# Performance work log

Hardware: AMD Instinct MI355X
Metric: run time of the kernel (lower is better)

## Reference

```python
import jax, jax.numpy as jnp
import numpy as np

HEADS = 8
DIM_HEAD = 64
LN_EPS = 1e-5


def _layernorm(x, gamma, beta):
    mu = jnp.mean(x, axis=-1, keepdims=True)
    var = jnp.var(x, axis=-1, keepdims=True)
    return (x - mu) * jax.lax.rsqrt(var + LN_EPS) * gamma + beta


def setup_inputs() -> dict:
    key = jax.random.key(0)
    ks = jax.random.split(key, 5)
    B, N, D = 1, 16384, 512
    return {
        "x": jax.random.normal(ks[0], (B, N, D), dtype=jnp.float32),
        "ln_gamma": jnp.ones((D,), dtype=jnp.float32),
        "ln_beta": jnp.zeros((D,), dtype=jnp.float32),
        "w_qkv": jax.random.normal(ks[1], (D, 3 * D), dtype=jnp.float32) * (D ** -0.5),
        "agent": jax.random.normal(ks[2], (HEADS, 512, DIM_HEAD), dtype=jnp.float32) * (DIM_HEAD ** -0.5),
        "w_out": jax.random.normal(ks[3], (D, D), dtype=jnp.float32) * (D ** -0.5),
        "b_out": jnp.zeros((D,), dtype=jnp.float32),
    }


def reference(x, ln_gamma, ln_beta, w_qkv, agent, w_out, b_out):
    # TransLayer: x + Mask_Agent_Attention(LayerNorm(x))
    B, N, D = x.shape
    xn = _layernorm(x, ln_gamma, ln_beta)

    qkv = xn @ w_qkv                                   # [B, N, 3D]
    q, k, v = jnp.split(qkv, 3, axis=-1)
    # [B, H, N, d]
    q = q.reshape(B, N, HEADS, DIM_HEAD).transpose(0, 2, 1, 3)
    k = k.reshape(B, N, HEADS, DIM_HEAD).transpose(0, 2, 1, 3)
    v = v.reshape(B, N, HEADS, DIM_HEAD).transpose(0, 2, 1, 3)

    scale = DIM_HEAD ** -0.5  # tem=0 -> classical 1/sqrt(d) scaling

    # agents aggregate values: softmax over keys  [B, H, A, N]
    attn1 = jax.nn.softmax(jnp.einsum('had,bhnd->bhan', agent, k) * scale, axis=-1)
    agent_v = jnp.einsum('bhan,bhnd->bhad', attn1, v)  # [B, H, A, d]

    # queries attend to agents: softmax over agents  [B, H, N, A]
    attn2 = jax.nn.softmax(jnp.einsum('bhnd,had->bhna', q, agent) * scale, axis=-1)
    out = jnp.einsum('bhna,bhad->bhnd', attn2, agent_v)  # [B, H, N, d]

    out = out + v  # residual=True: value residual inside attention
    out = out.transpose(0, 2, 1, 3).reshape(B, N, D)
    out = out @ w_out + b_out
    return x + out
```

## Files before the change

kernel.cpp:

```cpp
#include <hip/hip_runtime.h>
#include <stdint.h>

typedef unsigned short u16;
typedef __attribute__((ext_vector_type(8))) short bf16x8;
typedef __attribute__((ext_vector_type(4))) float f32x4;

__device__ __forceinline__ float bf2f(u16 u){
  union { uint32_t i; float f; } v; v.i = ((uint32_t)u) << 16; return v.f;
}
__device__ __forceinline__ u16 f2bf(float f){
  union { float fl; uint32_t i; } v; v.fl = f;
  uint32_t r = v.i + 0x7FFFu + ((v.i >> 16) & 1u);
  return (u16)(r >> 16);
}
__device__ __forceinline__ uint32_t cvt_pk_bf16(float lo, float hi){
  uint32_t r;
  asm("v_cvt_pk_bf16_f32 %0, %1, %2" : "=v"(r) : "v"(lo), "v"(hi));
  return r;
}
__device__ __forceinline__ f32x4 mfma16(bf16x8 a, bf16x8 b, f32x4 c){
  return __builtin_amdgcn_mfma_f32_16x16x32_bf16(a, b, c, 0, 0, 0);
}
__device__ __forceinline__ void gload16(const u16* g, u16* l){
  __builtin_amdgcn_global_load_lds((const __attribute__((address_space(1))) void*)g,
                                   (__attribute__((address_space(3))) void*)l, 16, 0, 0);
}

__global__ __launch_bounds__(256) void k_conv_bf(const float* __restrict__ in, u16* __restrict__ out, int n, float scale){
  int i = (blockIdx.x * 256 + threadIdx.x) * 4;
  if (i >= n) return;
  float4 v = *(const float4*)(in + i);
  ushort4 o; o.x=f2bf(v.x*scale); o.y=f2bf(v.y*scale); o.z=f2bf(v.z*scale); o.w=f2bf(v.w*scale);
  *(ushort4*)(out + i) = o;
}

__global__ __launch_bounds__(256) void k_transp(const float* __restrict__ in, u16* __restrict__ out, int R, int C){
  __shared__ u16 tile[64][68];
  int c0 = blockIdx.x * 64, r0 = blockIdx.y * 64;
  int tr = threadIdx.x >> 4;
  int tc = (threadIdx.x & 15) * 4;
  for (int rr = 0; rr < 4; rr++){
    int r = rr * 16 + tr;
    float4 v = *(const float4*)(in + (size_t)(r0 + r) * C + c0 + tc);
    ushort4 o; o.x=f2bf(v.x); o.y=f2bf(v.y); o.z=f2bf(v.z); o.w=f2bf(v.w);
    *(ushort4*)&tile[r][tc] = o;
  }
  __syncthreads();
  for (int rr = 0; rr < 4; rr++){
    int oc = rr * 16 + tr;
    ushort4 o;
    o.x = tile[tc+0][oc]; o.y = tile[tc+1][oc]; o.z = tile[tc+2][oc]; o.w = tile[tc+3][oc];
    *(ushort4*)(out + (size_t)(c0 + oc) * R + r0 + tc) = o;
  }
}

__global__ __launch_bounds__(256) void k_transp_v(const u16* __restrict__ qkv, u16* __restrict__ vT){
  __shared__ u16 tile[64][68];
  int n0 = blockIdx.x * 64;
  int c0 = blockIdx.y * 64;
  int tr = threadIdx.x >> 4;
  int tc = (threadIdx.x & 15) * 4;
  for (int rr = 0; rr < 4; rr++){
    int r = rr * 16 + tr;
    ushort4 v = *(const ushort4*)(qkv + (size_t)(n0 + r) * 1536 + 1024 + c0 + tc);
    *(ushort4*)&tile[r][tc] = v;
  }
  __syncthreads();
  for (int rr = 0; rr < 4; rr++){
    int oc = rr * 16 + tr;
    ushort4 o;
    o.x = tile[tc+0][oc]; o.y = tile[tc+1][oc]; o.z = tile[tc+2][oc]; o.w = tile[tc+3][oc];
    *(ushort4*)(vT + (size_t)(c0 + oc) * 16384 + n0 + tc) = o;
  }
}

__global__ __launch_bounds__(128) void k_ln(const float* __restrict__ x, const float* __restrict__ g,
                                            const float* __restrict__ b, u16* __restrict__ xn){
  int row = blockIdx.x;
  int t = threadIdx.x;
  float4 v = *(const float4*)(x + (size_t)row * 512 + t * 4);
  float s = v.x + v.y + v.z + v.w;
  float q = v.x*v.x + v.y*v.y + v.z*v.z + v.w*v.w;
  for (int o = 32; o > 0; o >>= 1){ s += __shfl_down(s, o); q += __shfl_down(q, o); }
  __shared__ float red[4];
  if ((t & 63) == 0){ red[(t >> 6) * 2] = s; red[(t >> 6) * 2 + 1] = q; }
  __syncthreads();
  float mu  = (red[0] + red[2]) * (1.0f/512.0f);
  float var = (red[1] + red[3]) * (1.0f/512.0f) - mu * mu;
  float rs = rsqrtf(var + 1e-5f);
  float4 gv = *(const float4*)(g + t * 4);
  float4 bv = *(const float4*)(b + t * 4);
  ushort4 o;
  o.x = f2bf((v.x - mu) * rs * gv.x + bv.x);
  o.y = f2bf((v.y - mu) * rs * gv.y + bv.y);
  o.z = f2bf((v.z - mu) * rs * gv.z + bv.z);
  o.w = f2bf((v.w - mu) * rs * gv.w + bv.w);
  *(ushort4*)(xn + (size_t)row * 512 + t * 4) = o;
}


__global__ __launch_bounds__(512) void k_gemm_qkv(const u16* __restrict__ A, const u16* __restrict__ Bt,
                                                  u16* __restrict__ C){
  __shared__ u16 aL[2][256 * 64];
  __shared__ u16 bL[2][128 * 64];
  int m0 = blockIdx.x * 256, n0 = blockIdx.y * 128;
  int t = threadIdx.x, w = t >> 6, l = t & 63;
  int wm = (w >> 1) * 64, wn = (w & 1) * 64;
  int lr = l & 15;
  int blkSrc = (l & 7) ^ ((l >> 3) & 7);
  const u16* gA = A  + (size_t)(m0 + w*8 + (l >> 3)) * 512 + blkSrc * 8;
  const u16* gB = Bt + (size_t)(n0 + w*8 + (l >> 3)) * 512 + blkSrc * 8;
  f32x4 acc[4][4];
  for (int i=0;i<4;i++) for (int j=0;j<4;j++) acc[i][j] = {0.f,0.f,0.f,0.f};

  auto stage = [&](int buf, int k0){
    #pragma unroll
    for (int p = 0; p < 4; p++)
      gload16(gA + (size_t)p*64*512 + k0, &aL[buf][(p*64 + w*8) * 64]);
    #pragma unroll
    for (int p = 0; p < 2; p++)
      gload16(gB + (size_t)p*64*512 + k0, &bL[buf][(p*64 + w*8) * 64]);
  };
  auto comp = [&](const u16* ab, const u16* bb){
    #pragma unroll
    for (int kk = 0; kk < 64; kk += 32){
      int xo = (((l >> 4) + (kk >> 3)) ^ (l & 7)) << 3;
      bf16x8 av[4], bv[4];
      #pragma unroll
      for (int mt=0;mt<4;mt++) av[mt] = *(const bf16x8*)&ab[(wm + mt*16 + lr)*64 + xo];
      #pragma unroll
      for (int nt=0;nt<4;nt++) bv[nt] = *(const bf16x8*)&bb[(wn + nt*16 + lr)*64 + xo];
      #pragma unroll
      for (int mt=0;mt<4;mt++)
        #pragma unroll
        for (int nt=0;nt<4;nt++)
          acc[mt][nt] = mfma16(av[mt], bv[nt], acc[mt][nt]);
    }
  };

  stage(0, 0);
  __syncthreads();
  #pragma unroll
  for (int tk = 0; tk < 8; tk++){
    int cur = tk & 1;
    if (tk < 7) stage(cur ^ 1, (tk + 1) * 64);
    comp(&aL[cur][0], &bL[cur][0]);
    __syncthreads();
  }

  int rr = (l >> 4) * 4, cc = l & 15;
  for (int mt=0;mt<4;mt++) for (int nt=0;nt<4;nt++)
    for (int j=0;j<4;j++){
      int r = m0 + wm + mt*16 + rr + j;
      int c = n0 + wn + nt*16 + cc;
      C[(size_t)r * 1536 + c] = f2bf(acc[mt][nt][j]);
    }
}

__global__ __launch_bounds__(512) void k_gemm_out(const u16* __restrict__ A, const u16* __restrict__ Bt,
                                                  const float* __restrict__ x, const float* __restrict__ bias,
                                                  float* __restrict__ y){
  __shared__ u16 aL[2][256 * 64];
  __shared__ u16 bL[2][128 * 64];
  int m0 = blockIdx.x * 256, n0 = blockIdx.y * 128;
  int t = threadIdx.x, w = t >> 6, l = t & 63;
  int wm = (w >> 1) * 64, wn = (w & 1) * 64;
  int lr = l & 15;
  int blkSrc = (l & 7) ^ ((l >> 3) & 7);
  const u16* gA = A  + (size_t)(m0 + w*8 + (l >> 3)) * 512 + blkSrc * 8;
  const u16* gB = Bt + (size_t)(n0 + w*8 + (l >> 3)) * 512 + blkSrc * 8;
  f32x4 acc[4][4];
  for (int i=0;i<4;i++) for (int j=0;j<4;j++) acc[i][j] = {0.f,0.f,0.f,0.f};

  auto stage = [&](int buf, int k0){
    #pragma unroll
    for (int p = 0; p < 4; p++)
      gload16(gA + (size_t)p*64*512 + k0, &aL[buf][(p*64 + w*8) * 64]);
    #pragma unroll
    for (int p = 0; p < 2; p++)
      gload16(gB + (size_t)p*64*512 + k0, &bL[buf][(p*64 + w*8) * 64]);
  };
  auto comp = [&](const u16* ab, const u16* bb){
    #pragma unroll
    for (int kk = 0; kk < 64; kk += 32){
      int xo = (((l >> 4) + (kk >> 3)) ^ (l & 7)) << 3;
      bf16x8 av[4], bv[4];
      #pragma unroll
      for (int mt=0;mt<4;mt++) av[mt] = *(const bf16x8*)&ab[(wm + mt*16 + lr)*64 + xo];
      #pragma unroll
      for (int nt=0;nt<4;nt++) bv[nt] = *(const bf16x8*)&bb[(wn + nt*16 + lr)*64 + xo];
      #pragma unroll
      for (int mt=0;mt<4;mt++)
        #pragma unroll
        for (int nt=0;nt<4;nt++)
          acc[mt][nt] = mfma16(av[mt], bv[nt], acc[mt][nt]);
    }
  };

  stage(0, 0);
  __syncthreads();
  #pragma unroll
  for (int tk = 0; tk < 8; tk++){
    int cur = tk & 1;
    if (tk < 7) stage(cur ^ 1, (tk + 1) * 64);
    comp(&aL[cur][0], &bL[cur][0]);
    __syncthreads();
  }

  int rr = (l >> 4) * 4, cc = l & 15;
  for (int mt=0;mt<4;mt++) for (int nt=0;nt<4;nt++)
    for (int j=0;j<4;j++){
      int r = m0 + wm + mt*16 + rr + j;
      int c = n0 + wn + nt*16 + cc;
      y[(size_t)r * 512 + c] = acc[mt][nt][j] + bias[c] + x[(size_t)r * 512 + c];
    }
}

__global__ __launch_bounds__(256) void k_agent_agg(const u16* __restrict__ agbf, const u16* __restrict__ qkv,
                                                   const u16* __restrict__ vT,
                                                   float* __restrict__ nump, float* __restrict__ denp){
  int L = blockIdx.x;
  int g = (L >> 6) * 8 + (L & 7);
  int m = (L >> 3) & 7;
  int h = g >> 4, ch = g & 15, a0 = m * 64;

  __shared__ u16 ag[64][72];
  __shared__ u16 kt[64][72];
  __shared__ u16 vt[64][72];
  __shared__ u16 pt[64][72];
  int t = threadIdx.x, w = t >> 6, l = t & 63;

  for (int i = 0; i < 2; i++){
    int flat = t + 256 * i;
    int r = flat >> 3, c = (flat & 7) * 8;
    *(uint4*)&ag[r][c] = *(const uint4*)(agbf + (size_t)(h * 512 + a0 + r) * 64 + c);
  }

  bf16x8 ones;
  for (int i = 0; i < 8; i++) ones[i] = (short)0x3F80;

  f32x4 acc2[4];
  for (int i=0;i<4;i++) acc2[i] = {0.f,0.f,0.f,0.f};
  f32x4 accd = {0.f,0.f,0.f,0.f};

  for (int sub = 0; sub < 16; sub++){
    int n0 = ch * 1024 + sub * 64;
    __syncthreads();
    {
      int flat = t;
      int r = flat >> 3, c = (flat & 7) * 8;
      *(uint4*)&kt[r][c] = *(const uint4*)(qkv + (size_t)(n0 + r) * 1536 + 512 + h * 64 + c);
      int flat2 = t + 256;
      int r2 = flat2 >> 3, c2 = (flat2 & 7) * 8;
      *(uint4*)&kt[r2][c2] = *(const uint4*)(qkv + (size_t)(n0 + r2) * 1536 + 512 + h * 64 + c2);
      *(uint4*)&vt[r][c]   = *(const uint4*)(vT + ((size_t)(h * 64 + r) << 14) + n0 + c);
      *(uint4*)&vt[r2][c2] = *(const uint4*)(vT + ((size_t)(h * 64 + r2) << 14) + n0 + c2);
    }
    __syncthreads();

    f32x4 s[4];
    for (int nt=0;nt<4;nt++) s[nt] = {0.f,0.f,0.f,0.f};
    for (int kk = 0; kk < 64; kk += 32){
      int kb = kk + (l >> 4) * 8;
      bf16x8 kf = *(const bf16x8*)&kt[w*16 + (l & 15)][kb];
      for (int nt=0;nt<4;nt++){
        bf16x8 af = *(const bf16x8*)&ag[nt*16 + (l & 15)][kb];
        s[nt] = mfma16(kf, af, s[nt]);
      }
    }
    int nb = w*16 + (l >> 4) * 4;
    for (int nt=0;nt<4;nt++){
      int a = nt*16 + (l & 15);
      uint32_t w0 = cvt_pk_bf16(__builtin_amdgcn_exp2f(s[nt][0]), __builtin_amdgcn_exp2f(s[nt][1]));
      uint32_t w1 = cvt_pk_bf16(__builtin_amdgcn_exp2f(s[nt][2]), __builtin_amdgcn_exp2f(s[nt][3]));
      uint2 o; o.x = w0; o.y = w1;
      *(uint2*)&pt[a][nb] = o;
    }
    __syncthreads();

    for (int kk = 0; kk < 64; kk += 32){
      int kb = kk + (l >> 4) * 8;
      bf16x8 vf = *(const bf16x8*)&vt[w*16 + (l & 15)][kb];
      for (int mt=0;mt<4;mt++){
        bf16x8 pf = *(const bf16x8*)&pt[mt*16 + (l & 15)][kb];
        acc2[mt] = mfma16(pf, vf, acc2[mt]);
      }
      bf16x8 pw = *(const bf16x8*)&pt[w*16 + (l & 15)][kb];
      accd = mfma16(ones, pw, accd);
    }
  }

  size_t base = ((size_t)(h * 16 + ch) * 512 + a0) * 64;
  for (int mt=0;mt<4;mt++)
    #pragma unroll
    for (int j=0;j<4;j++){
      int a = mt*16 + (l>>4)*4 + j;
      int d = w*16 + (l&15);
      nump[base + (size_t)a*64 + d] = acc2[mt][j];
    }
  if (l < 16) denp[(size_t)(h*16 + ch) * 512 + a0 + w*16 + l] = accd[0];
}

__global__ __launch_bounds__(64) void k_agent_reduce(const float* __restrict__ nump, const float* __restrict__ denp,
                                                     u16* __restrict__ avtg){
  int h = blockIdx.x >> 9;
  int a = blockIdx.x & 511;
  int d = threadIdx.x;
  float num = 0.f, den = 0.f;
  for (int c = 0; c < 16; c++){
    num += nump[((size_t)(h * 16 + c) * 512 + a) * 64 + d];
    den += denp[(size_t)(h * 16 + c) * 512 + a];
  }
  avtg[((size_t)h * 64 + d) * 512 + a] = f2bf(num / den);
}

__global__ __launch_bounds__(256) void k_qattn(const u16* __restrict__ qkv, const u16* __restrict__ agbf,
                                               const u16* __restrict__ avtg, u16* __restrict__ atto){
  int n0 = blockIdx.x * 64;
  int h  = blockIdx.y;
  __shared__ u16 pt[64][72];
  __shared__ float dnf[64];
  int t = threadIdx.x, w = t >> 6, l = t & 63;
  int lr = l & 15, q4 = l >> 4;

  bf16x8 qf[4][2];
  #pragma unroll
  for (int nt=0;nt<4;nt++)
    #pragma unroll
    for (int kk=0;kk<2;kk++)
      qf[nt][kk] = *(const bf16x8*)(qkv + (size_t)(n0 + nt*16 + lr) * 1536 + h*64 + kk*32 + q4*8);

  bf16x8 ones;
  #pragma unroll
  for (int i = 0; i < 8; i++) ones[i] = (short)0x3F80;

  const u16* agp = agbf + (size_t)(h*512 + w*16 + lr) * 64;
  const u16* avp = avtg + (size_t)(h*64  + w*16 + lr) * 512;

  f32x4 acc[4];
  #pragma unroll
  for (int i=0;i<4;i++) acc[i] = {0.f,0.f,0.f,0.f};
  f32x4 accd = {0.f,0.f,0.f,0.f};

  for (int at = 0; at < 8; at++){
    int a0 = at * 64;

    f32x4 s[4];
    #pragma unroll
    for (int nt=0;nt<4;nt++) s[nt] = {0.f,0.f,0.f,0.f};
    #pragma unroll
    for (int kk = 0; kk < 2; kk++){
      bf16x8 af = *(const bf16x8*)(agp + (size_t)a0*64 + kk*32 + q4*8);
      #pragma unroll
      for (int nt=0;nt<4;nt++)
        s[nt] = mfma16(af, qf[nt][kk], s[nt]);
    }

    __syncthreads();
    int ab = w*16 + q4*4;
    #pragma unroll
    for (int nt=0;nt<4;nt++){
      int n = nt*16 + lr;
      uint32_t w0 = cvt_pk_bf16(__builtin_amdgcn_exp2f(s[nt][0]), __builtin_amdgcn_exp2f(s[nt][1]));
      uint32_t w1 = cvt_pk_bf16(__builtin_amdgcn_exp2f(s[nt][2]), __builtin_amdgcn_exp2f(s[nt][3]));
      uint2 o; o.x = w0; o.y = w1;
      *(uint2*)&pt[n][ab] = o;
    }
    __syncthreads();

    #pragma unroll
    for (int kk = 0; kk < 64; kk += 32){
      int kb = kk + q4*8;
      bf16x8 vf = *(const bf16x8*)(avp + a0 + kb);
      #pragma unroll
      for (int mt=0;mt<4;mt++){
        bf16x8 pf = *(const bf16x8*)&pt[mt*16 + lr][kb];
        acc[mt] = mfma16(pf, vf, acc[mt]);
      }
      bf16x8 pw = *(const bf16x8*)&pt[w*16 + lr][kb];
      accd = mfma16(ones, pw, accd);
    }
  }

  if (l < 16) dnf[w*16 + l] = accd[0];
  __syncthreads();
  if (t < 64) dnf[t] = __builtin_amdgcn_rcpf(dnf[t]);
  __syncthreads();

  int d = w*16 + lr;
  #pragma unroll
  for (int mt=0;mt<4;mt++){
    #pragma unroll
    for (int j=0;j<4;j++){
      int n = mt*16 + q4*4 + j;
      float v = bf2f(qkv[(size_t)(n0 + n) * 1536 + 1024 + h * 64 + d]);
      atto[(size_t)(n0 + n) * 512 + h * 64 + d] = f2bf(acc[mt][j] * dnf[n] + v);
    }
  }
}

extern "C" void kernel_launch(void* const* d_in, const int* in_sizes, int n_in,
                              void* d_out, int out_size, void* d_ws, size_t ws_size,
                              hipStream_t stream) {
  const float* x     = (const float*)d_in[0];
  const float* gamma = (const float*)d_in[1];
  const float* beta  = (const float*)d_in[2];
  const float* w_qkv = (const float*)d_in[3];
  const float* agent = (const float*)d_in[4];
  const float* w_out = (const float*)d_in[5];
  const float* b_out = (const float*)d_in[6];
  float* y = (float*)d_out;

  char* ws = (char*)d_ws;
  u16*   xn    = (u16*)  (ws + 0);
  u16*   vT    = (u16*)  (ws + 0);
  u16*   qkv   = (u16*)  (ws + 16777216);
  u16*   wqkvt = (u16*)  (ws + 67108864);
  u16*   woutt = (u16*)  (ws + 68681728);
  u16*   agbf  = (u16*)  (ws + 69206016);
  u16*   avtg  = (u16*)  (ws + 69730304);
  u16*   atto  = (u16*)  (ws + 70254592);
  float* nump  = (float*)(ws + 87031808);
  float* denp  = (float*)(ws + 103809024);

  k_conv_bf   <<<dim3(256),     dim3(256), 0, stream>>>(agent, agbf, 8*512*64, 0.125f * 1.44269504089f);
  k_transp    <<<dim3(24, 8),   dim3(256), 0, stream>>>(w_qkv, wqkvt, 512, 1536);
  k_transp    <<<dim3(8, 8),    dim3(256), 0, stream>>>(w_out, woutt, 512, 512);
  k_ln        <<<dim3(16384),   dim3(128), 0, stream>>>(x, gamma, beta, xn);
  k_gemm_qkv  <<<dim3(64, 12),  dim3(512), 0, stream>>>(xn, wqkvt, qkv);
  k_transp_v  <<<dim3(256, 8),  dim3(256), 0, stream>>>(qkv, vT);
  k_agent_agg <<<dim3(1024),    dim3(256), 0, stream>>>(agbf, qkv, vT, nump, denp);
  k_agent_reduce<<<dim3(4096),  dim3(64),  0, stream>>>(nump, denp, avtg);
  k_qattn     <<<dim3(256, 8),  dim3(256), 0, stream>>>(qkv, agbf, avtg, atto);
  k_gemm_out  <<<dim3(64, 4),   dim3(512), 0, stream>>>(atto, woutt, x, b_out, y);
}
```

Baseline: 171.4 us.

## Fuse V transpose into QKV GEMM epilogue and pipeline agent tiles in qattn

Removes the separate V-transpose kernel by having the QKV GEMM epilogue also write transposed V tiles for the V column blocks. The query-attention kernel now stages agent and agent-value tiles in double-buffered shared memory with register prefetch. It overlaps the PV MFMA of the previous tile with the score computation of the current one. It also replaces the ones-vector MFMA denominator with per-lane sums reduced by shuffles. vT now aliases the atto region, which is safe only because vT is consumed before atto is written. The change adds extra LDS traffic and narrow scattered stores in the GEMM epilogue.

Result: faster. 160.0 us (-6.6%).

```diff
diff --git a/kernel.cpp b/kernel.cpp
--- a/kernel.cpp
+++ b/kernel.cpp
@@ -51,26 +51,6 @@
     ushort4 o;
     o.x = tile[tc+0][oc]; o.y = tile[tc+1][oc]; o.z = tile[tc+2][oc]; o.w = tile[tc+3][oc];
     *(ushort4*)(out + (size_t)(c0 + oc) * R + r0 + tc) = o;
-  }
-}
-
-__global__ __launch_bounds__(256) void k_transp_v(const u16* __restrict__ qkv, u16* __restrict__ vT){
-  __shared__ u16 tile[64][68];
-  int n0 = blockIdx.x * 64;
-  int c0 = blockIdx.y * 64;
-  int tr = threadIdx.x >> 4;
-  int tc = (threadIdx.x & 15) * 4;
-  for (int rr = 0; rr < 4; rr++){
-    int r = rr * 16 + tr;
-    ushort4 v = *(const ushort4*)(qkv + (size_t)(n0 + r) * 1536 + 1024 + c0 + tc);
-    *(ushort4*)&tile[r][tc] = v;
-  }
-  __syncthreads();
-  for (int rr = 0; rr < 4; rr++){
-    int oc = rr * 16 + tr;
-    ushort4 o;
-    o.x = tile[tc+0][oc]; o.y = tile[tc+1][oc]; o.z = tile[tc+2][oc]; o.w = tile[tc+3][oc];
-    *(ushort4*)(vT + (size_t)(c0 + oc) * 16384 + n0 + tc) = o;
   }
 }
 
@@ -98,9 +78,8 @@
   *(ushort4*)(xn + (size_t)row * 512 + t * 4) = o;
 }
 
-
 __global__ __launch_bounds__(512) void k_gemm_qkv(const u16* __restrict__ A, const u16* __restrict__ Bt,
-                                                  u16* __restrict__ C){
+                                                  u16* __restrict__ C, u16* __restrict__ vT){
   __shared__ u16 aL[2][256 * 64];
   __shared__ u16 bL[2][128 * 64];
   int m0 = blockIdx.x * 256, n0 = blockIdx.y * 128;
@@ -149,12 +128,19 @@
   }
 
   int rr = (l >> 4) * 4, cc = l & 15;
-  for (int mt=0;mt<4;mt++) for (int nt=0;nt<4;nt++)
-    for (int j=0;j<4;j++){
-      int r = m0 + wm + mt*16 + rr + j;
-      int c = n0 + wn + nt*16 + cc;
-      C[(size_t)r * 1536 + c] = f2bf(acc[mt][nt][j]);
-    }
+  bool isV = (n0 >= 1024);
+  for (int mt=0;mt<4;mt++) for (int nt=0;nt<4;nt++){
+    int r = m0 + wm + mt*16 + rr;
+    int c = n0 + wn + nt*16 + cc;
+    ushort4 o;
+    o.x = f2bf(acc[mt][nt][0]); o.y = f2bf(acc[mt][nt][1]);
+    o.z = f2bf(acc[mt][nt][2]); o.w = f2bf(acc[mt][nt][3]);
+    C[(size_t)(r+0) * 1536 + c] = o.x;
+    C[(size_t)(r+1) * 1536 + c] = o.y;
+    C[(size_t)(r+2) * 1536 + c] = o.z;
+    C[(size_t)(r+3) * 1536 + c] = o.w;
+    if (isV) *(ushort4*)(vT + ((size_t)(c - 1024) << 14) + r) = o;
+  }
 }
 
 __global__ __launch_bounds__(512) void k_gemm_out(const u16* __restrict__ A, const u16* __restrict__ Bt,
@@ -318,8 +304,10 @@
                                                const u16* __restrict__ avtg, u16* __restrict__ atto){
   int n0 = blockIdx.x * 64;
   int h  = blockIdx.y;
-  __shared__ u16 pt[64][72];
-  __shared__ float dnf[64];
+  __shared__ u16 agL[2][64][68];
+  __shared__ u16 avL[2][64][68];
+  __shared__ u16 pt[2][64][68];
+  __shared__ float dnf[4][64];
   int t = threadIdx.x, w = t >> 6, l = t & 63;
   int lr = l & 15, q4 = l >> 4;
 
@@ -330,61 +318,101 @@
     for (int kk=0;kk<2;kk++)
       qf[nt][kk] = *(const bf16x8*)(qkv + (size_t)(n0 + nt*16 + lr) * 1536 + h*64 + kk*32 + q4*8);
 
-  bf16x8 ones;
-  #pragma unroll
-  for (int i = 0; i < 8; i++) ones[i] = (short)0x3F80;
-
-  const u16* agp = agbf + (size_t)(h*512 + w*16 + lr) * 64;
-  const u16* avp = avtg + (size_t)(h*64  + w*16 + lr) * 512;
+  int sr = t >> 2, sc = (t & 3) * 16;
+  uint4 rg0, rg1, rv0, rv1;
+  rg0 = *(const uint4*)(agbf + (size_t)(h*512 + sr) * 64 + sc);
+  rg1 = *(const uint4*)(agbf + (size_t)(h*512 + sr) * 64 + sc + 8);
+  rv0 = *(const uint4*)(avtg + (size_t)(h*64 + sr) * 512 + sc);
+  rv1 = *(const uint4*)(avtg + (size_t)(h*64 + sr) * 512 + sc + 8);
+  *(uint4*)&agL[0][sr][sc]     = rg0;
+  *(uint4*)&agL[0][sr][sc + 8] = rg1;
+  *(uint4*)&avL[0][sr][sc]     = rv0;
+  *(uint4*)&avL[0][sr][sc + 8] = rv1;
+  __syncthreads();
 
   f32x4 acc[4];
   #pragma unroll
   for (int i=0;i<4;i++) acc[i] = {0.f,0.f,0.f,0.f};
-  f32x4 accd = {0.f,0.f,0.f,0.f};
+  float den[4] = {0.f,0.f,0.f,0.f};
 
   for (int at = 0; at < 8; at++){
-    int a0 = at * 64;
-
+    int cur = at & 1, prv = cur ^ 1;
+    if (at + 1 < 8){
+      rg0 = *(const uint4*)(agbf + (size_t)(h*512 + (at+1)*64 + sr) * 64 + sc);
+      rg1 = *(const uint4*)(agbf + (size_t)(h*512 + (at+1)*64 + sr) * 64 + sc + 8);
+      rv0 = *(const uint4*)(avtg + (size_t)(h*64 + sr) * 512 + (at+1)*64 + sc);
+      rv1 = *(const uint4*)(avtg + (size_t)(h*64 + sr) * 512 + (at+1)*64 + sc + 8);
+    }
     f32x4 s[4];
     #pragma unroll
     for (int nt=0;nt<4;nt++) s[nt] = {0.f,0.f,0.f,0.f};
     #pragma unroll
     for (int kk = 0; kk < 2; kk++){
-      bf16x8 af = *(const bf16x8*)(agp + (size_t)a0*64 + kk*32 + q4*8);
+      bf16x8 af = *(const bf16x8*)&agL[cur][w*16 + lr][kk*32 + q4*8];
       #pragma unroll
       for (int nt=0;nt<4;nt++)
         s[nt] = mfma16(af, qf[nt][kk], s[nt]);
     }
-
-    __syncthreads();
-    int ab = w*16 + q4*4;
     #pragma unroll
     for (int nt=0;nt<4;nt++){
-      int n = nt*16 + lr;
-      uint32_t w0 = cvt_pk_bf16(__builtin_amdgcn_exp2f(s[nt][0]), __builtin_amdgcn_exp2f(s[nt][1]));
-      uint32_t w1 = cvt_pk_bf16(__builtin_amdgcn_exp2f(s[nt][2]), __builtin_amdgcn_exp2f(s[nt][3]));
-      uint2 o; o.x = w0; o.y = w1;
-      *(uint2*)&pt[n][ab] = o;
-    }
-    __syncthreads();
-
+      float e0 = __builtin_amdgcn_exp2f(s[nt][0]);
+      float e1 = __builtin_amdgcn_exp2f(s[nt][1]);
+      float e2 = __builtin_amdgcn_exp2f(s[nt][2]);
+      float e3 = __builtin_amdgcn_exp2f(s[nt][3]);
+      den[nt] += (e0 + e1) + (e2 + e3);
+      uint2 o; o.x = cvt_pk_bf16(e0, e1); o.y = cvt_pk_bf16(e2, e3);
+      *(uint2*)&pt[cur][nt*16 + lr][w*16 + q4*4] = o;
+    }
+    if (at > 0){
+      #pragma unroll
+      for (int kk = 0; kk < 64; kk += 32){
+        int kb = kk + q4*8;
+        bf16x8 vf = *(const bf16x8*)&avL[prv][w*16 + lr][kb];
+        #pragma unroll
+        for (int mt=0;mt<4;mt++){
+          bf16x8 pf = *(const bf16x8*)&pt[prv][mt*16 + lr][kb];
+          acc[mt] = mfma16(pf, vf, acc[mt]);
+        }
+      }
+    }
+    __syncthreads();
+    if (at + 1 < 8){
+      *(uint4*)&agL[prv][sr][sc]     = rg0;
+      *(uint4*)&agL[prv][sr][sc + 8] = rg1;
+      *(uint4*)&avL[prv][sr][sc]     = rv0;
+      *(uint4*)&avL[prv][sr][sc + 8] = rv1;
+    }
+    __syncthreads();
+  }
+  {
     #pragma unroll
     for (int kk = 0; kk < 64; kk += 32){
       int kb = kk + q4*8;
-      bf16x8 vf = *(const bf16x8*)(avp + a0 + kb);
+      bf16x8 vf = *(const bf16x8*)&avL[1][w*16 + lr][kb];
       #pragma unroll
       for (int mt=0;mt<4;mt++){
-        bf16x8 pf = *(const bf16x8*)&pt[mt*16 + lr][kb];
+        bf16x8 pf = *(const bf16x8*)&pt[1][mt*16 + lr][kb];
         acc[mt] = mfma16(pf, vf, acc[mt]);
       }
-      bf16x8 pw = *(const bf16x8*)&pt[w*16 + lr][kb];
-      accd = mfma16(ones, pw, accd);
-    }
-  }
-
-  if (l < 16) dnf[w*16 + l] = accd[0];
-  __syncthreads();
-  if (t < 64) dnf[t] = __builtin_amdgcn_rcpf(dnf[t]);
+    }
+  }
+
+  float dq[4];
+  #pragma unroll
+  for (int nt=0;nt<4;nt++){
+    float r = den[nt];
+    r += __shfl_xor(r, 16);
+    r += __shfl_xor(r, 32);
+    dq[nt] = r;
+  }
+  if (q4 == 0)
+    #pragma unroll
+    for (int nt=0;nt<4;nt++) dnf[w][nt*16 + lr] = dq[nt];
+  __syncthreads();
+  if (t < 64){
+    float sden = dnf[0][t] + dnf[1][t] + dnf[2][t] + dnf[3][t];
+    dnf[0][t] = __builtin_amdgcn_rcpf(sden);
+  }
   __syncthreads();
 
   int d = w*16 + lr;
@@ -394,7 +422,7 @@
     for (int j=0;j<4;j++){
       int n = mt*16 + q4*4 + j;
       float v = bf2f(qkv[(size_t)(n0 + n) * 1536 + 1024 + h * 64 + d]);
-      atto[(size_t)(n0 + n) * 512 + h * 64 + d] = f2bf(acc[mt][j] * dnf[n] + v);
+      atto[(size_t)(n0 + n) * 512 + h * 64 + d] = f2bf(acc[mt][j] * dnf[0][n] + v);
     }
   }
 }
@@ -413,12 +441,12 @@
 
   char* ws = (char*)d_ws;
   u16*   xn    = (u16*)  (ws + 0);
-  u16*   vT    = (u16*)  (ws + 0);
   u16*   qkv   = (u16*)  (ws + 16777216);
   u16*   wqkvt = (u16*)  (ws + 67108864);
   u16*   woutt = (u16*)  (ws + 68681728);
   u16*   agbf  = (u16*)  (ws + 69206016);
   u16*   avtg  = (u16*)  (ws + 69730304);
+  u16*   vT    = (u16*)  (ws + 70254592);
   u16*   atto  = (u16*)  (ws + 70254592);
   float* nump  = (float*)(ws + 87031808);
   float* denp  = (float*)(ws + 103809024);
@@ -427,8 +455,7 @@
   k_transp    <<<dim3(24, 8),   dim3(256), 0, stream>>>(w_qkv, wqkvt, 512, 1536);
   k_transp    <<<dim3(8, 8),    dim3(256), 0, stream>>>(w_out, woutt, 512, 512);
   k_ln        <<<dim3(16384),   dim3(128), 0, stream>>>(x, gamma, beta, xn);
-  k_gemm_qkv  <<<dim3(64, 12),  dim3(512), 0, stream>>>(xn, wqkvt, qkv);
-  k_transp_v  <<<dim3(256, 8),  dim3(256), 0, stream>>>(qkv, vT);
+  k_gemm_qkv  <<<dim3(64, 12),  dim3(512), 0, stream>>>(xn, wqkvt, qkv, vT);
   k_agent_agg <<<dim3(1024),    dim3(256), 0, stream>>>(agbf, qkv, vT, nump, denp);
   k_agent_reduce<<<dim3(4096),  dim3(64),  0, stream>>>(nump, denp, avtg);
   k_qattn     <<<dim3(256, 8),  dim3(256), 0, stream>>>(qkv, agbf, avtg, atto);
```
